# Kernel optimization log

Hardware: AMD Instinct MI355X
Metric: run time of the kernel (lower is better)

The kernel has to match this reference:

```python
import jax, jax.numpy as jnp
import numpy as np

BETA = 0.25
EPS = 1e-12  # matches F.normalize eps


def l2norm(t):
    n = jnp.sqrt(jnp.sum(t * t, axis=-1, keepdims=True))
    return t / jnp.maximum(n, EPS)


def setup_inputs() -> dict:
    key = jax.random.key(0)
    k1, k2 = jax.random.split(key)
    z = jax.random.normal(k1, (8, 256, 32, 32), dtype=jnp.float32)
    codebook = jax.random.normal(k2, (16384, 256), dtype=jnp.float32)
    return {"z": z, "codebook": codebook}


def reference(z, codebook):
    sg = jax.lax.stop_gradient
    b, c, h, w = z.shape
    zt = jnp.transpose(z, (0, 2, 3, 1))            # b h w c
    zf = l2norm(zt.reshape(-1, c))                 # [B*H*W, D], L2-normalized
    cb = l2norm(codebook)                          # [N, D], L2-normalized
    # squared euclidean distance between normalized vectors
    d = (jnp.sum(zf * zf, axis=1, keepdims=True)
         + jnp.sum(cb * cb, axis=1)
         - 2.0 * jnp.einsum('bd,nd->bn', zf, cb))  # [B*H*W, N]
    encoding_indices = jnp.argmin(d, axis=1)       # [B*H*W]
    # gather uses RAW (unnormalized) codebook, as nn.Embedding does
    z_q = codebook[encoding_indices].reshape(zt.shape)  # b h w c
    loss = BETA * jnp.mean((sg(z_q) - zt) ** 2) + jnp.mean((z_q - sg(zt)) ** 2)
    z_q_out = zt + sg(z_q - zt)                    # straight-through
    z_q_out = jnp.transpose(z_q_out, (0, 3, 1, 2)) # b c h w
    return loss, z_q_out, encoding_indices
```

## Files before the change

kernel.cpp:

```cpp
#include <hip/hip_runtime.h>
#include <float.h>
#include <math.h>

#define ZM 8192
#define CN 16384
#define KD 256
#define HWN 1024
#define ZSTRIDE 262144
#define NCHA 16

typedef short  s16x8  __attribute__((ext_vector_type(8)));
typedef float  f32x4  __attribute__((ext_vector_type(4)));

__device__ inline void gld_lds16(const void* g, void* l) {
    __builtin_amdgcn_global_load_lds((__attribute__((address_space(1))) void*)(g),
                                     (__attribute__((address_space(3))) void*)(l), 16, 0, 0);
}


__global__ void cbprep_kernel(const float* __restrict__ cb, float* __restrict__ cbrinv,
                              float* __restrict__ cbsq, __bf16* __restrict__ Bh) {
    __shared__ float sm[4];
    __shared__ float rsh;
    int n = blockIdx.x;
    float v = cb[(size_t)n * KD + threadIdx.x];
    float s = v * v;
    #pragma unroll
    for (int m = 32; m; m >>= 1) s += __shfl_xor(s, m, 64);
    if ((threadIdx.x & 63) == 0) sm[threadIdx.x >> 6] = s;
    __syncthreads();
    if (threadIdx.x == 0) {
        float t = sm[0] + sm[1] + sm[2] + sm[3];
        float r = 1.0f / fmaxf(sqrtf(t), 1e-12f);
        cbrinv[n] = r;
        cbsq[n] = t * r * r;
        rsh = r;
    }
    __syncthreads();
    Bh[(size_t)n * KD + threadIdx.x] = (__bf16)(v * rsh);
}


__global__ void prep_a_kernel(const float* __restrict__ z, __bf16* __restrict__ Ah,
                              float* __restrict__ Zt) {
    __shared__ float tile[64][65];
    int hw0 = blockIdx.x * 64, c0 = blockIdx.y * 64, b = blockIdx.z;
    int tid = threadIdx.x;
    #pragma unroll
    for (int i = 0; i < 16; ++i) {
        int lin = i * 256 + tid;
        int cl = lin >> 6, hwl = lin & 63;
        tile[cl][hwl] = z[(size_t)b * ZSTRIDE + (size_t)(c0 + cl) * HWN + hw0 + hwl];
    }
    __syncthreads();
    #pragma unroll
    for (int i = 0; i < 16; ++i) {
        int lin = i * 256 + tid;
        int hwl = lin >> 6, cl = lin & 63;
        float v = tile[cl][hwl];
        size_t o = (size_t)(b * 1024 + hw0 + hwl) * KD + c0 + cl;
        Ah[o] = (__bf16)v;
        Zt[o] = v;
    }
}


__global__ __launch_bounds__(256, 2) void gemm_top2_kernel(
    const __bf16* __restrict__ A, const __bf16* __restrict__ B,
    uint2* __restrict__ part)
{
    __shared__ __bf16 sA[128 * 64];
    __shared__ __bf16 sB[128 * 64];
    __shared__ uint2 sred[2][128];

    const int tid = threadIdx.x;
    const int l = tid & 63;
    const int wid = tid >> 6;
    const int wm = (wid >> 1) * 64, wn = (wid & 1) * 64;
    const int m0 = blockIdx.x * 128;
    const int chunk = blockIdx.y;
    const int fr = l & 15;
    const int fkg = l >> 4;

    int laneOff[4], dstOff[4];
    #pragma unroll
    for (int j = 0; j < 4; ++j) {
        int sl = j * 256 + tid;
        int r = sl >> 3, c = sl & 7;
        int cs = c ^ (r & 7);
        laneOff[j] = r * KD + cs * 8;
        dstOff[j] = sl * 8;
    }

    const int cg0 = fkg ^ (fr & 7);
    const int fA0 = (wm + fr) * 64 + cg0 * 8;
    const int fB0 = (wn + fr) * 64 + cg0 * 8;

    unsigned khi[16], klo[16];
    #pragma unroll
    for (int sx = 0; sx < 16; ++sx) { khi[sx] = 0u; klo[sx] = 0u; }

    f32x4 acc[4][4];
    #pragma unroll
    for (int ti = 0; ti < 4; ++ti)
        #pragma unroll
        for (int tj = 0; tj < 4; ++tj) acc[ti][tj] = (f32x4){0.f, 0.f, 0.f, 0.f};

    const __bf16* Ac = A + (size_t)m0 * KD;
    const __bf16* Bc = B + (size_t)chunk * 1024 * KD;

    for (int s = 0; s < 32; ++s) {
        #pragma unroll
        for (int j = 0; j < 4; ++j) {
            gld_lds16(Ac + laneOff[j], &sA[dstOff[j]]);
            gld_lds16(Bc + laneOff[j], &sB[dstOff[j]]);
        }
        if ((s & 3) == 3) { Ac -= 192; Bc += 128 * KD - 192; }
        else              { Ac += 64;  Bc += 64; }
        __syncthreads();

        #pragma unroll
        for (int kh = 0; kh < 2; ++kh) {
            const __bf16* fB = &sB[fB0 ^ (kh * 32)];
            const __bf16* fA = &sA[fA0 ^ (kh * 32)];
            s16x8 bhf[4];
            #pragma unroll
            for (int tj = 0; tj < 4; ++tj)
                bhf[tj] = *(const s16x8*)(fB + tj * 1024);
            #pragma unroll
            for (int ti = 0; ti < 4; ++ti) {
                s16x8 ahf = *(const s16x8*)(fA + ti * 1024);
                #pragma unroll
                for (int tj = 0; tj < 4; ++tj)
                    acc[ti][tj] = __builtin_amdgcn_mfma_f32_16x16x32_bf16(ahf, bhf[tj], acc[ti][tj], 0, 0, 0);
            }
        }

        if ((s & 3) == 3) {
            const int t = s >> 2;
            #pragma unroll
            for (int sx = 0; sx < 16; ++sx) {
                const int ti = sx >> 2, r = sx & 3;
                #pragma unroll
                for (int tj = 0; tj < 4; ++tj) {
                    unsigned u = __float_as_uint(acc[ti][tj][r]);
                    u ^= ((unsigned)((int)u >> 31)) | 0x80000000u;
                    unsigned key = (u & 0xFFFFFC00u) | (unsigned)(t * 128 + wn + tj * 16 + fr);
                    unsigned h = khi[sx];
                    unsigned mn = min(h, key);
                    khi[sx] = max(h, key);
                    klo[sx] = max(klo[sx], mn);
                    acc[ti][tj][r] = 0.f;
                }
            }
        }
        __syncthreads();
    }

    #pragma unroll
    for (int sx = 0; sx < 16; ++sx) {
        unsigned h = khi[sx], lo_ = klo[sx];
        #pragma unroll
        for (int m = 1; m < 16; m <<= 1) {
            unsigned oh = (unsigned)__shfl_xor((int)h, m, 64);
            unsigned ol = (unsigned)__shfl_xor((int)lo_, m, 64);
            unsigned nh = max(h, oh);
            lo_ = max(min(h, oh), max(lo_, ol));
            h = nh;
        }
        if ((l & 15) == 0) {
            int rowlb = wm + (sx >> 2) * 16 + (l >> 4) * 4 + (sx & 3);
            sred[wn >> 6][rowlb] = make_uint2(h, lo_);
        }
    }
    __syncthreads();
    if (tid < 128) {
        uint2 pa = sred[0][tid], pb = sred[1][tid];
        unsigned h = max(pa.x, pb.x);
        unsigned lo_ = max(min(pa.x, pb.x), max(pa.y, pb.y));
        part[(size_t)(m0 + tid) * NCHA + chunk] = make_uint2(h, lo_);
    }
}


__global__ void rescue_all_kernel(const float* __restrict__ Zt, const float* __restrict__ cb,
                                  const float* __restrict__ cbrinv, const float* __restrict__ cbsq,
                                  const uint2* __restrict__ part,
                                  int* __restrict__ ridx, float* __restrict__ out_idx) {
    int row = blockIdx.x;
    __shared__ float zrow[KD];
    int tid = threadIdx.x;
    ((float4*)zrow)[tid] = ((const float4*)(Zt + (size_t)row * KD))[tid];
    __syncthreads();

    float tot = 0.f;
    #pragma unroll
    for (int w = 0; w < 4; ++w) {
        float v = zrow[w * 64 + tid];
        float s = v * v;
        #pragma unroll
        for (int m = 32; m; m >>= 1) s += __shfl_xor(s, m, 64);
        tot += s;
    }
    float zrinv = 1.0f / fmaxf(sqrtf(tot), 1e-12f);

    int slot = tid & 31;
    uint2 p = part[(size_t)row * NCHA + (slot >> 1)];
    unsigned key = (slot & 1) ? p.y : p.x;
    int n = (slot >> 1) * 1024 + (int)(key & 1023u);
    float sc = cbrinv[n];
    const float4* c4 = (const float4*)(cb + (size_t)n * KD);
    const float4* z4 = (const float4*)zrow;
    float acc = 0.f;
    #pragma unroll 8
    for (int k = 0; k < KD / 4; ++k) {
        float4 cv = c4[k];
        float4 zv = z4[k];
        acc = fmaf(zv.x, cv.x * sc, acc);
        acc = fmaf(zv.y, cv.y * sc, acc);
        acc = fmaf(zv.z, cv.z * sc, acc);
        acc = fmaf(zv.w, cv.w * sc, acc);
    }
    float s = fmaf(zrinv, acc, -0.5f * cbsq[n]);
    #pragma unroll
    for (int m = 1; m < 32; m <<= 1) {
        float ov = __shfl_xor(s, m, 64); int on = __shfl_xor(n, m, 64);
        if (ov > s || (ov == s && on < n)) { s = ov; n = on; }
    }
    if (tid == 0) { ridx[row] = n; out_idx[row] = (float)n; }
}


__global__ void finalize_kernel(const float* __restrict__ Zt, const float* __restrict__ cb,
                                const int* __restrict__ ridx,
                                float* __restrict__ zq_out, float* __restrict__ lpart) {
    __shared__ float zqt[16][257];
    __shared__ int idxs[16];
    __shared__ float sm[4];
    int b = blockIdx.x, hw0 = blockIdx.y * 16, tid = threadIdx.x;
    if (tid < 16) idxs[tid] = ridx[b * 1024 + hw0 + tid];
    __syncthreads();
    int w = tid >> 6, ln = tid & 63;
    int c0 = ln * 4;
    float dsum = 0.f;
    #pragma unroll
    for (int j = 0; j < 4; ++j) {
        int rl = w * 4 + j;
        int row = b * 1024 + hw0 + rl;
        float4 zt4 = *(const float4*)&Zt[(size_t)row * KD + c0];
        float4 cv  = *(const float4*)&cb[(size_t)idxs[rl] * KD + c0];
        float d0 = cv.x - zt4.x, d1 = cv.y - zt4.y;
        float d2 = cv.z - zt4.z, d3 = cv.w - zt4.w;
        zqt[rl][c0 + 0] = zt4.x + d0;
        zqt[rl][c0 + 1] = zt4.y + d1;
        zqt[rl][c0 + 2] = zt4.z + d2;
        zqt[rl][c0 + 3] = zt4.w + d3;
        dsum = fmaf(d0, d0, dsum);
        dsum = fmaf(d1, d1, dsum);
        dsum = fmaf(d2, d2, dsum);
        dsum = fmaf(d3, d3, dsum);
    }
    #pragma unroll
    for (int m = 32; m; m >>= 1) dsum += __shfl_xor(dsum, m, 64);
    if ((tid & 63) == 0) sm[tid >> 6] = dsum;
    __syncthreads();
    if (tid == 0) lpart[b * 64 + blockIdx.y] = sm[0] + sm[1] + sm[2] + sm[3];
    #pragma unroll
    for (int it = 0; it < 16; ++it) {
        int idx = it * 256 + tid;
        int c = idx >> 4, hwl = idx & 15;
        zq_out[(size_t)b * ZSTRIDE + (size_t)c * HWN + hw0 + hwl] = zqt[hwl][c];
    }
}

__global__ void loss_final_kernel(const float* __restrict__ lpart, float* __restrict__ out) {
    __shared__ float sm[4];
    float s = 0.0f;
    for (int i = threadIdx.x; i < 512; i += 256) s += lpart[i];
    #pragma unroll
    for (int m = 32; m; m >>= 1) s += __shfl_xor(s, m, 64);
    if ((threadIdx.x & 63) == 0) sm[threadIdx.x >> 6] = s;
    __syncthreads();
    if (threadIdx.x == 0) {
        float total = sm[0] + sm[1] + sm[2] + sm[3];
        float m = total * (1.0f / 2097152.0f);
        out[0] = fmaf(0.25f, m, m);
    }
}


extern "C" void kernel_launch(void* const* d_in, const int* in_sizes, int n_in,
                              void* d_out, int out_size, void* d_ws, size_t ws_size,
                              hipStream_t stream) {
    const float* z  = (const float*)d_in[0];
    const float* cb = (const float*)d_in[1];
    float* out = (float*)d_out;

    float* ws = (float*)d_ws;
    float*  cbrinv = ws;
    float*  cbsq   = cbrinv + CN;
    int*    ridx   = (int*)(cbsq + CN);
    float*  lpart  = (float*)(ridx + ZM);
    uint2*  part   = (uint2*)(lpart + ZM);
    __bf16* Ah     = (__bf16*)(part + (size_t)ZM * NCHA);
    __bf16* Bh     = Ah + (size_t)ZM * KD;
    float*  Zt     = (float*)(Bh + (size_t)CN * KD);

    float* out_loss = out;
    float* out_zq   = out + 1;
    float* out_idx  = out + 1 + (size_t)ZM * KD;

    cbprep_kernel<<<CN, 256, 0, stream>>>(cb, cbrinv, cbsq, Bh);
    prep_a_kernel<<<dim3(16, 4, 8), 256, 0, stream>>>(z, Ah, Zt);
    gemm_top2_kernel<<<dim3(64, 16), 256, 0, stream>>>(Ah, Bh, part);
    rescue_all_kernel<<<ZM, 64, 0, stream>>>(Zt, cb, cbrinv, cbsq, part, ridx, out_idx);
    finalize_kernel<<<dim3(8, 64), 256, 0, stream>>>(Zt, cb, ridx, out_zq, lpart);
    loss_final_kernel<<<1, 256, 0, stream>>>(lpart, out_loss);
}
```

Baseline: 179.5 us.

## Skip fp32 rescue when top-2 margin is large; fuse prep kernels

Result: faster. 145.6 us, median of 3 (-18.9%).

```diff
diff --git a/kernel.cpp b/kernel.cpp
--- a/kernel.cpp
+++ b/kernel.cpp
@@ -8,6 +8,7 @@
 #define HWN 1024
 #define ZSTRIDE 262144
 #define NCHA 16
+#define TAU 0.125f
 
 typedef short  s16x8  __attribute__((ext_vector_type(8)));
 typedef float  f32x4  __attribute__((ext_vector_type(4)));
@@ -18,49 +19,49 @@
 }
 
 
-__global__ void cbprep_kernel(const float* __restrict__ cb, float* __restrict__ cbrinv,
-                              float* __restrict__ cbsq, __bf16* __restrict__ Bh) {
-    __shared__ float sm[4];
-    __shared__ float rsh;
-    int n = blockIdx.x;
-    float v = cb[(size_t)n * KD + threadIdx.x];
-    float s = v * v;
-    #pragma unroll
-    for (int m = 32; m; m >>= 1) s += __shfl_xor(s, m, 64);
-    if ((threadIdx.x & 63) == 0) sm[threadIdx.x >> 6] = s;
-    __syncthreads();
-    if (threadIdx.x == 0) {
-        float t = sm[0] + sm[1] + sm[2] + sm[3];
-        float r = 1.0f / fmaxf(sqrtf(t), 1e-12f);
-        cbrinv[n] = r;
-        cbsq[n] = t * r * r;
-        rsh = r;
-    }
-    __syncthreads();
-    Bh[(size_t)n * KD + threadIdx.x] = (__bf16)(v * rsh);
-}
-
-
-__global__ void prep_a_kernel(const float* __restrict__ z, __bf16* __restrict__ Ah,
-                              float* __restrict__ Zt) {
+__global__ void prep_fused_kernel(const float* __restrict__ cb, const float* __restrict__ z,
+                                  float* __restrict__ cbrinv, float* __restrict__ cbsq,
+                                  __bf16* __restrict__ Bh, __bf16* __restrict__ Ah,
+                                  float* __restrict__ Zt) {
     __shared__ float tile[64][65];
-    int hw0 = blockIdx.x * 64, c0 = blockIdx.y * 64, b = blockIdx.z;
-    int tid = threadIdx.x;
-    #pragma unroll
-    for (int i = 0; i < 16; ++i) {
-        int lin = i * 256 + tid;
-        int cl = lin >> 6, hwl = lin & 63;
-        tile[cl][hwl] = z[(size_t)b * ZSTRIDE + (size_t)(c0 + cl) * HWN + hw0 + hwl];
-    }
-    __syncthreads();
-    #pragma unroll
-    for (int i = 0; i < 16; ++i) {
-        int lin = i * 256 + tid;
-        int hwl = lin >> 6, cl = lin & 63;
-        float v = tile[cl][hwl];
-        size_t o = (size_t)(b * 1024 + hw0 + hwl) * KD + c0 + cl;
-        Ah[o] = (__bf16)v;
-        Zt[o] = v;
+    int bid = blockIdx.x, tid = threadIdx.x;
+    if (bid < CN) {
+        float* sm = &tile[0][0];
+        int n = bid;
+        float v = cb[(size_t)n * KD + tid];
+        float s = v * v;
+        #pragma unroll
+        for (int m = 32; m; m >>= 1) s += __shfl_xor(s, m, 64);
+        if ((tid & 63) == 0) sm[tid >> 6] = s;
+        __syncthreads();
+        if (tid == 0) {
+            float t = sm[0] + sm[1] + sm[2] + sm[3];
+            float r = 1.0f / fmaxf(sqrtf(t), 1e-12f);
+            cbrinv[n] = r;
+            cbsq[n] = t * r * r;
+            sm[4] = r;
+        }
+        __syncthreads();
+        Bh[(size_t)n * KD + tid] = (__bf16)(v * sm[4]);
+    } else {
+        int pid = bid - CN;
+        int hw0 = (pid & 15) * 64, c0 = ((pid >> 4) & 3) * 64, b = pid >> 6;
+        #pragma unroll
+        for (int i = 0; i < 16; ++i) {
+            int lin = i * 256 + tid;
+            int cl = lin >> 6, hwl = lin & 63;
+            tile[cl][hwl] = z[(size_t)b * ZSTRIDE + (size_t)(c0 + cl) * HWN + hw0 + hwl];
+        }
+        __syncthreads();
+        #pragma unroll
+        for (int i = 0; i < 16; ++i) {
+            int lin = i * 256 + tid;
+            int hwl = lin >> 6, cl = lin & 63;
+            float v = tile[cl][hwl];
+            size_t o = (size_t)(b * 1024 + hw0 + hwl) * KD + c0 + cl;
+            Ah[o] = (__bf16)v;
+            Zt[o] = v;
+        }
     }
 }
 
@@ -104,7 +105,7 @@
     #pragma unroll
     for (int ti = 0; ti < 4; ++ti)
         #pragma unroll
-        for (int tj = 0; tj < 4; ++tj) acc[ti][tj] = (f32x4){0.f, 0.f, 0.f, 0.f};
+        for (int tj = 0; tj < 4; ++tj) acc[ti][tj] = (f32x4){32.f, 32.f, 32.f, 32.f};
 
     const __bf16* Ac = A + (size_t)m0 * KD;
     const __bf16* Bc = B + (size_t)chunk * 1024 * KD;
@@ -144,13 +145,12 @@
                 #pragma unroll
                 for (int tj = 0; tj < 4; ++tj) {
                     unsigned u = __float_as_uint(acc[ti][tj][r]);
-                    u ^= ((unsigned)((int)u >> 31)) | 0x80000000u;
                     unsigned key = (u & 0xFFFFFC00u) | (unsigned)(t * 128 + wn + tj * 16 + fr);
                     unsigned h = khi[sx];
                     unsigned mn = min(h, key);
                     khi[sx] = max(h, key);
                     klo[sx] = max(klo[sx], mn);
-                    acc[ti][tj][r] = 0.f;
+                    acc[ti][tj][r] = 32.f;
                 }
             }
         }
@@ -183,13 +183,32 @@
 }
 
 
-__global__ void rescue_all_kernel(const float* __restrict__ Zt, const float* __restrict__ cb,
+__global__ void rescue_sel_kernel(const float* __restrict__ Zt, const float* __restrict__ cb,
                                   const float* __restrict__ cbrinv, const float* __restrict__ cbsq,
                                   const uint2* __restrict__ part,
                                   int* __restrict__ ridx, float* __restrict__ out_idx) {
     int row = blockIdx.x;
+    int tid = threadIdx.x;
+    const uint2* p = part + (size_t)row * NCHA;
+
+    unsigned b1 = 0u, b2 = 0u;
+    int c1 = 0;
+    #pragma unroll
+    for (int c = 0; c < NCHA; ++c) {
+        uint2 q = p[c];
+        if (q.x > b1) {
+            b2 = (b1 > q.y) ? b1 : q.y;
+            b1 = q.x; c1 = c;
+        } else if (q.x > b2) { b2 = q.x; }
+    }
+    float gap = __uint_as_float(b1 & 0xFFFFFC00u) - __uint_as_float(b2 & 0xFFFFFC00u);
+    int n1 = c1 * 1024 + (int)(b1 & 1023u);
+    if (gap >= TAU) {
+        if (tid == 0) { ridx[row] = n1; out_idx[row] = (float)n1; }
+        return;
+    }
+
     __shared__ float zrow[KD];
-    int tid = threadIdx.x;
     ((float4*)zrow)[tid] = ((const float4*)(Zt + (size_t)row * KD))[tid];
     __syncthreads();
 
@@ -205,8 +224,8 @@
     float zrinv = 1.0f / fmaxf(sqrtf(tot), 1e-12f);
 
     int slot = tid & 31;
-    uint2 p = part[(size_t)row * NCHA + (slot >> 1)];
-    unsigned key = (slot & 1) ? p.y : p.x;
+    uint2 q = p[slot >> 1];
+    unsigned key = (slot & 1) ? q.y : q.x;
     int n = (slot >> 1) * 1024 + (int)(key & 1023u);
     float sc = cbrinv[n];
     const float4* c4 = (const float4*)(cb + (size_t)n * KD);
@@ -310,10 +329,9 @@
     float* out_zq   = out + 1;
     float* out_idx  = out + 1 + (size_t)ZM * KD;
 
-    cbprep_kernel<<<CN, 256, 0, stream>>>(cb, cbrinv, cbsq, Bh);
-    prep_a_kernel<<<dim3(16, 4, 8), 256, 0, stream>>>(z, Ah, Zt);
+    prep_fused_kernel<<<CN + 512, 256, 0, stream>>>(cb, z, cbrinv, cbsq, Bh, Ah, Zt);
     gemm_top2_kernel<<<dim3(64, 16), 256, 0, stream>>>(Ah, Bh, part);
-    rescue_all_kernel<<<ZM, 64, 0, stream>>>(Zt, cb, cbrinv, cbsq, part, ridx, out_idx);
+    rescue_sel_kernel<<<ZM, 64, 0, stream>>>(Zt, cb, cbrinv, cbsq, part, ridx, out_idx);
     finalize_kernel<<<dim3(8, 64), 256, 0, stream>>>(Zt, cb, ridx, out_zq, lpart);
     loss_final_kernel<<<1, 256, 0, stream>>>(lpart, out_loss);
 }
```
